# Optimization experiments

Measured on AMD Instinct MI355X. Metric: run time of the kernel, lower is better.

## Reference

```python
import jax, jax.numpy as jnp
import numpy as np
import math

D = 768      # d_model
H = 12       # heads
DH = D // H  # per-head dim
HID = 3072   # ffn hidden
L = 6        # layers each for encoder/decoder
S = 1024     # encoder seq len
T = 1024     # decoder seq len
MAXLEN = 1024


def pos_encoding(d, length):
    # pe[pos, 2i] = sin(pos / scale**i), pe[pos, 2i+1] = cos(pos / scale**i), scale = 1000**(2/d)
    scale = 1000.0 ** (2.0 / d)
    inv = scale ** (-np.arange(d // 2, dtype=np.float64))
    ang = np.arange(length, dtype=np.float64)[:, None] * inv[None, :]
    pe = np.zeros((length, d), dtype=np.float32)
    pe[:, 0::2] = np.sin(ang)
    pe[:, 1::2] = np.cos(ang)
    return jnp.asarray(pe)


def setup_inputs() -> dict:
    key = jax.random.key(0)
    ks = iter(jax.random.split(key, 64))
    def nrm(shape, s=0.02):
        return jax.random.normal(next(ks), shape, dtype=jnp.float32) * s
    inp = {
        'xl': nrm((S, D), 1.0),
        'dl': nrm((T, D), 1.0),
        'pos_enc': pos_encoding(D, MAXLEN),
        # encoder params (stacked over L layers, heads stacked over H)
        'enc_wq': nrm((L, H, DH, D)), 'enc_wk': nrm((L, H, DH, D)), 'enc_wv': nrm((L, H, DH, D)),
        'enc_wo': nrm((L, D, D)), 'enc_bo': jnp.zeros((L, D), jnp.float32),
        'enc_ln_a': jnp.ones((L, 2, D), jnp.float32), 'enc_ln_b': jnp.zeros((L, 2, D), jnp.float32),
        'enc_w1': nrm((L, HID, D)), 'enc_b1': jnp.zeros((L, HID), jnp.float32),
        'enc_w2': nrm((L, D, HID)), 'enc_b2': jnp.zeros((L, D), jnp.float32),
        # decoder self-attention
        'dec_wq': nrm((L, H, DH, D)), 'dec_wk': nrm((L, H, DH, D)), 'dec_wv': nrm((L, H, DH, D)),
        'dec_wo': nrm((L, D, D)), 'dec_bo': jnp.zeros((L, D), jnp.float32),
        # decoder cross-attention
        'dec_cwq': nrm((L, H, DH, D)), 'dec_cwk': nrm((L, H, DH, D)), 'dec_cwv': nrm((L, H, DH, D)),
        'dec_cwo': nrm((L, D, D)), 'dec_cbo': jnp.zeros((L, D), jnp.float32),
        'dec_ln_a': jnp.ones((L, 3, D), jnp.float32), 'dec_ln_b': jnp.zeros((L, 3, D), jnp.float32),
        'dec_w1': nrm((L, HID, D)), 'dec_b1': jnp.zeros((L, HID), jnp.float32),
        'dec_w2': nrm((L, D, HID)), 'dec_b2': jnp.zeros((L, D), jnp.float32),
    }
    return inp


def _ln_res(x, fx, a, b, eps=1e-6):
    # x = x + fx; a*(x-mean)/(std+eps)+b with UNBIASED std (torch default) and std (not var) in denom
    x = x + fx
    m = x.mean(-1, keepdims=True)
    s = jnp.std(x, axis=-1, keepdims=True, ddof=1)
    return a * (x - m) / (s + eps) + b


def _mha(qx, kx, vx, wq, wk, wv, wo, bo, mask=None):
    q = jnp.einsum('sd,hed->hse', qx, wq)  # [H,S,dh]
    k = jnp.einsum('td,hed->hte', kx, wk)
    v = jnp.einsum('td,hed->hte', vx, wv)
    scores = jnp.einsum('hse,hte->hst', q, k) / math.sqrt(q.shape[-1])
    if mask is not None:
        scores = scores + mask
    p = jax.nn.softmax(scores, axis=-1)  # softmax over keys (torch dim=1 on 2D scores)
    o = jnp.einsum('hst,hte->hse', p, v)
    o = jnp.transpose(o, (1, 0, 2)).reshape(qx.shape[0], -1)  # concat heads
    return o @ wo.T + bo


def _ffn(x, w1, b1, w2, b2):
    return jax.nn.relu(x @ w1.T + b1) @ w2.T + b2


def reference(xl, dl, pos_enc, enc_wq, enc_wk, enc_wv, enc_wo, enc_bo, enc_ln_a, enc_ln_b,
              enc_w1, enc_b1, enc_w2, enc_b2,
              dec_wq, dec_wk, dec_wv, dec_wo, dec_bo,
              dec_cwq, dec_cwk, dec_cwv, dec_cwo, dec_cbo,
              dec_ln_a, dec_ln_b, dec_w1, dec_b1, dec_w2, dec_b2):
    m = xl + pos_enc[: xl.shape[0]]
    for l in range(L):
        fx = _mha(m, m, m, enc_wq[l], enc_wk[l], enc_wv[l], enc_wo[l], enc_bo[l])
        m = _ln_res(m, fx, enc_ln_a[l, 0], enc_ln_b[l, 0])
        fx = _ffn(m, enc_w1[l], enc_b1[l], enc_w2[l], enc_b2[l])
        m = _ln_res(m, fx, enc_ln_a[l, 1], enc_ln_b[l, 1])
    n = dl.shape[0]
    # additive causal mask: -10000 where j > i
    cmask = -10000.0 * (jnp.arange(n)[None, :] > jnp.arange(n)[:, None]).astype(jnp.float32)
    out = dl + pos_enc[:n]
    for l in range(L):
        fx = _mha(out, out, out, dec_wq[l], dec_wk[l], dec_wv[l], dec_wo[l], dec_bo[l], cmask)
        out = _ln_res(out, fx, dec_ln_a[l, 0], dec_ln_b[l, 0])
        fx = _mha(out, m, m, dec_cwq[l], dec_cwk[l], dec_cwv[l], dec_cwo[l], dec_cbo[l])
        out = _ln_res(out, fx, dec_ln_a[l, 1], dec_ln_b[l, 1])
        fx = _ffn(out, dec_w1[l], dec_b1[l], dec_w2[l], dec_b2[l])
        out = _ln_res(out, fx, dec_ln_a[l, 2], dec_ln_b[l, 2])
    return jax.nn.softmax(out, axis=1)
```

## Files before the change

### kernel.cpp

```cpp
#include <hip/hip_runtime.h>
#include <math.h>

#define DMODEL 768
#define NHEAD 12
#define DHEAD 64
#define HIDDEN 3072
#define NLAYER 6
#define SEQ 1024
#define AC_ELEMS (SEQ * DMODEL)

typedef unsigned short u16;
typedef __attribute__((ext_vector_type(8))) short short8;
typedef __attribute__((ext_vector_type(4))) float f32x4;

__device__ __forceinline__ u16 f2bf(float f) {
    union { float f; unsigned u; } v; v.f = f;
    unsigned u = v.u;
    return (u16)((u + 0x7fffu + ((u >> 16) & 1u)) >> 16);
}
__device__ __forceinline__ float bf2f(u16 b) {
    union { unsigned u; float f; } v; v.u = ((unsigned)b) << 16; return v.f;
}

__device__ __forceinline__ void async16(const void* g, void* l) {
    __builtin_amdgcn_global_load_lds(
        (const __attribute__((address_space(1))) unsigned int*)g,
        (__attribute__((address_space(3))) unsigned int*)l, 16, 0, 0);
}

template<int N> __device__ __forceinline__ void waitv() {
    asm volatile("s_waitcnt vmcnt(%0)" :: "n"(N) : "memory");
    __builtin_amdgcn_sched_barrier(0);
}
__device__ __forceinline__ void drain_all() {
    asm volatile("s_waitcnt vmcnt(0) lgkmcnt(0)" ::: "memory");
    __builtin_amdgcn_sched_barrier(0);
}
__device__ __forceinline__ void bar() {
    __builtin_amdgcn_sched_barrier(0);
    __builtin_amdgcn_s_barrier();
    __builtin_amdgcn_sched_barrier(0);
}

__device__ __forceinline__ float block_sum(float v, float* red) {
    int tid = threadIdx.x;
    red[tid] = v;
    __syncthreads();
#pragma unroll
    for (int s = 128; s > 0; s >>= 1) {
        if (tid < s) red[tid] += red[tid + s];
        __syncthreads();
    }
    float r = red[0];
    __syncthreads();
    return r;
}
__device__ __forceinline__ float block_max(float v, float* red) {
    int tid = threadIdx.x;
    red[tid] = v;
    __syncthreads();
#pragma unroll
    for (int s = 128; s > 0; s >>= 1) {
        if (tid < s) red[tid] = fmaxf(red[tid], red[tid + s]);
        __syncthreads();
    }
    float r = red[0];
    __syncthreads();
    return r;
}

__global__ __launch_bounds__(256) void add_pe(const float* __restrict__ a,
                                              const float* __restrict__ b,
                                              float* __restrict__ o,
                                              u16* __restrict__ ob, int n) {
    int i = blockIdx.x * 256 + threadIdx.x;
    if (i < n) { float v = a[i] + b[i]; o[i] = v; ob[i] = f2bf(v); }
}

__global__ __launch_bounds__(256) void cvt_bf16(const float* __restrict__ src,
                                                u16* __restrict__ dst,
                                                long long per, long long sls, long long dls) {
    long long i = ((long long)blockIdx.x * 256 + threadIdx.x) * 4;
    if (i >= per) return;
    const float* s = src + (long long)blockIdx.y * sls + i;
    u16* d = dst + (long long)blockIdx.y * dls + i;
    float4 v = *(const float4*)s;
    ushort4 o;
    o.x = f2bf(v.x); o.y = f2bf(v.y); o.z = f2bf(v.z); o.w = f2bf(v.w);
    *(ushort4*)d = o;
}

template<int TM, int TN, int WR, int WC>
__global__ __launch_bounds__(WR * WC * 64) void gemm_mfma(
    const u16* __restrict__ A, int lda,
    const void* __restrict__ Bp, int ldb, int b_f32,
    const float* __restrict__ bias,
    void* __restrict__ Cp, int ldc, int c_bf16,
    float* __restrict__ C2,
    u16* __restrict__ vt_out, int vt_col0,
    int Ksub, int relu)
{
    constexpr int T  = WR * WC * 64;
    constexpr bool MW = (WR * WC) > 1;
    constexpr int FM = TM / (WR * 16), FN = TN / (WC * 16);
    constexpr int NA = TM * 8 / T, NB = TN * 8 / T;
    constexpr int LPS = NA + NB;
    __shared__ __align__(16) u16 As[3][TM * 64];
    __shared__ __align__(16) u16 Bs[3][TN * 64];

    const int zs = blockIdx.z;
    const u16*   B16 = (const u16*)Bp   + (long long)zs * Ksub;
    const float* B32 = (const float*)Bp + (long long)zs * Ksub;
    A += (long long)zs * Ksub;
    u16*   C16 = (u16*)Cp;
    float* C32 = (float*)Cp;

    const int t = threadIdx.x, lane = t & 63, w = t >> 6;
    const int wy = w / WC, wx = w % WC;
    const int n0 = blockIdx.y * TM, m0 = blockIdx.x * TN;

    auto stage = [&](int b, int k0) {
#pragma unroll
        for (int i = 0; i < NA; ++i) {
            int L = i * T + t;
            int row = L >> 3, cp = L & 7, c = cp ^ (row & 7);
            async16(A + (long long)(n0 + row) * lda + k0 + (c << 3),
                    &As[b][(i * T + w * 64) * 8]);
        }
        if (!b_f32) {
#pragma unroll
            for (int i = 0; i < NB; ++i) {
                int L = i * T + t;
                int row = L >> 3, cp = L & 7, c = cp ^ (row & 7);
                async16(B16 + (long long)(m0 + row) * ldb + k0 + (c << 3),
                        &Bs[b][(i * T + w * 64) * 8]);
            }
        } else {
#pragma unroll
            for (int i = 0; i < NB; ++i) {
                int L = i * T + t;
                int row = L >> 3, cp = L & 7, c = cp ^ (row & 7);
                const float* s = B32 + (long long)(m0 + row) * ldb + k0 + (c << 3);
                float4 x = *(const float4*)s;
                float4 y = *(const float4*)(s + 4);
                uint4 pk;
                pk.x = (unsigned)f2bf(x.x) | ((unsigned)f2bf(x.y) << 16);
                pk.y = (unsigned)f2bf(x.z) | ((unsigned)f2bf(x.w) << 16);
                pk.z = (unsigned)f2bf(y.x) | ((unsigned)f2bf(y.y) << 16);
                pk.w = (unsigned)f2bf(y.z) | ((unsigned)f2bf(y.w) << 16);
                *(uint4*)&Bs[b][row * 64 + cp * 8] = pk;
            }
        }
    };

    const int nk = Ksub / 64;
    stage(0, 0);
    if (nk > 1) stage(1, 64);

    f32x4 acc[FM][FN] = {};

    for (int tt = 0; tt < nk; ++tt) {
        if (tt + 2 < nk) stage((tt + 2) % 3, (tt + 2) * 64);
        if (b_f32)             drain_all();
        else if (tt + 2 < nk)  waitv<2 * LPS>();
        else if (tt + 1 < nk)  waitv<LPS>();
        else                   waitv<0>();
        if (MW) bar();

        const u16* Ac = As[tt % 3];
        const u16* Bc = Bs[tt % 3];
#pragma unroll
        for (int kk = 0; kk < 2; ++kk) {
            short8 af[FM], bfv[FN];
            const int cb = kk * 4 + (lane >> 4);
#pragma unroll
            for (int m = 0; m < FM; ++m) {
                int R = wy * (TM / WR) + m * 16 + (lane & 15);
                af[m] = *(const short8*)&Ac[R * 64 + ((cb ^ (R & 7)) << 3)];
            }
#pragma unroll
            for (int n = 0; n < FN; ++n) {
                int R = wx * (TN / WC) + n * 16 + (lane & 15);
                bfv[n] = *(const short8*)&Bc[R * 64 + ((cb ^ (R & 7)) << 3)];
            }
#pragma unroll
            for (int m = 0; m < FM; ++m)
#pragma unroll
                for (int n = 0; n < FN; ++n)
                    acc[m][n] = __builtin_amdgcn_mfma_f32_16x16x32_bf16(af[m], bfv[n], acc[m][n], 0, 0, 0);
        }
        if (MW) bar();
    }

    const int cj = lane & 15, ci0 = (lane >> 4) << 2;
    const bool z0 = (zs == 0);
#pragma unroll
    for (int m = 0; m < FM; ++m) {
#pragma unroll
        for (int n = 0; n < FN; ++n) {
            int col = m0 + wx * (TN / WC) + n * 16 + cj;
            bool to_vt = z0 && vt_out && (col >= vt_col0);
            float bv = (z0 && bias) ? bias[col] : 0.0f;
#pragma unroll
            for (int r = 0; r < 4; ++r) {
                int row = n0 + wy * (TM / WR) + m * 16 + ci0 + r;
                float v = acc[m][n][r] + bv;
                if (relu) v = fmaxf(v, 0.0f);
                if (!z0)          C2[(long long)row * ldc + col] = v;
                else if (to_vt)   vt_out[(long long)(col - vt_col0) * SEQ + row] = f2bf(v);
                else if (c_bf16)  C16[(long long)row * ldc + col] = f2bf(v);
                else              C32[(long long)row * ldc + col] = v;
            }
        }
    }
}

template<int CAUSAL>
__global__ __launch_bounds__(256) void attn_split(
    const u16* __restrict__ Qg,
    const u16* __restrict__ Kg,
    const u16* __restrict__ VT,
    float* __restrict__ Op,
    float* __restrict__ Ml)
{
    const int h  = blockIdx.y;
    const int qt = blockIdx.x;
    const int s  = blockIdx.z;
    const int q0 = qt * 64;
    const int t = threadIdx.x, lane = t & 63, w = t >> 6;

    const int last = CAUSAL ? qt : (SEQ / 64 - 1);

    if (CAUSAL && s > last) {
        for (int e = t; e < 64 * 64; e += 256) {
            int r = e >> 6, c = e & 63;
            Op[(long long)s * AC_ELEMS + (long long)(q0 + r) * DMODEL + h * 64 + c] = 0.0f;
        }
        if (t < 64) {
            long long mi = (((long long)s * NHEAD + h) * SEQ + q0 + t) * 2;
            Ml[mi] = -3.0e38f; Ml[mi + 1] = 0.0f;
        }
        return;
    }

    __shared__ __align__(16) u16 Ks[2][64 * 64];
    __shared__ __align__(16) u16 Vs[2][64 * 64];
    __shared__ __align__(16) u16 Ps[4][16 * 64];

    short8 qf[2];
    {
        int qrow = q0 + w * 16 + (lane & 15);
        const u16* qp = Qg + (long long)qrow * (3 * DMODEL) + h * DHEAD + ((lane >> 4) << 3);
        qf[0] = *(const short8*)qp;
        qf[1] = *(const short8*)(qp + 32);
    }

    auto stage = [&](int b, int kt) {
#pragma unroll
        for (int i = 0; i < 2; ++i) {
            int LL = i * 256 + t;
            int row = LL >> 3, cp = LL & 7, c = cp ^ (row & 7);
            async16(Kg + (long long)(kt * 64 + row) * (3 * DMODEL) + h * DHEAD + (c << 3),
                    &Ks[b][(i * 256 + w * 64) * 8]);
            async16(VT + (long long)(h * DHEAD + row) * SEQ + kt * 64 + (c << 3),
                    &Vs[b][(i * 256 + w * 64) * 8]);
        }
    };

    f32x4 o_acc[4] = {};
    float m_r[4], l_r[4];
#pragma unroll
    for (int r = 0; r < 4; ++r) { m_r[r] = -3.0e38f; l_r[r] = 0.f; }

    stage(0, s);

    int buf = 0;
    for (int kt = s; kt <= last; kt += 2) {
        if (kt + 2 <= last) { stage(buf ^ 1, kt + 2); waitv<4>(); }
        else                { waitv<0>(); }
        bar();

        f32x4 sv[4] = {};
#pragma unroll
        for (int kk = 0; kk < 2; ++kk) {
            const int cb = kk * 4 + (lane >> 4);
#pragma unroll
            for (int n = 0; n < 4; ++n) {
                int R = n * 16 + (lane & 15);
                short8 kf = *(const short8*)&Ks[buf][R * 64 + ((cb ^ (R & 7)) << 3)];
                sv[n] = __builtin_amdgcn_mfma_f32_16x16x32_bf16(qf[kk], kf, sv[n], 0, 0, 0);
            }
        }

#pragma unroll
        for (int n = 0; n < 4; ++n) {
            int keyl = n * 16 + (lane & 15);
#pragma unroll
            for (int r = 0; r < 4; ++r) {
                float v = sv[n][r] * 0.125f;
                if (CAUSAL && kt == qt) {
                    int ql = w * 16 + ((lane >> 4) << 2) + r;
                    if (keyl > ql) v -= 10000.0f;
                }
                sv[n][r] = v;
            }
        }

#pragma unroll
        for (int r = 0; r < 4; ++r) {
            float vm = fmaxf(fmaxf(sv[0][r], sv[1][r]), fmaxf(sv[2][r], sv[3][r]));
            vm = fmaxf(vm, __shfl_xor(vm, 1));
            vm = fmaxf(vm, __shfl_xor(vm, 2));
            vm = fmaxf(vm, __shfl_xor(vm, 4));
            vm = fmaxf(vm, __shfl_xor(vm, 8));
            float mn = fmaxf(m_r[r], vm);
            float sf = __expf(m_r[r] - mn);
            m_r[r] = mn;
            float rowsum = 0.f;
#pragma unroll
            for (int n = 0; n < 4; ++n) {
                float p = __expf(sv[n][r] - mn);
                sv[n][r] = p;
                rowsum += p;
            }
            rowsum += __shfl_xor(rowsum, 1);
            rowsum += __shfl_xor(rowsum, 2);
            rowsum += __shfl_xor(rowsum, 4);
            rowsum += __shfl_xor(rowsum, 8);
            l_r[r] = l_r[r] * sf + rowsum;
#pragma unroll
            for (int d = 0; d < 4; ++d) o_acc[d][r] *= sf;
        }

#pragma unroll
        for (int n = 0; n < 4; ++n) {
            int jh = lane & 7;
            int chunk = n * 2 + ((lane & 15) >> 3);
#pragma unroll
            for (int r = 0; r < 4; ++r) {
                int q = ((lane >> 4) << 2) + r;
                Ps[w][q * 64 + ((chunk ^ (q & 7)) << 3) + jh] = f2bf(sv[n][r]);
            }
        }

#pragma unroll
        for (int kk = 0; kk < 2; ++kk) {
            int q = lane & 15;
            int chunk = (lane >> 4) + kk * 4;
            short8 pf = *(const short8*)&Ps[w][q * 64 + ((chunk ^ (q & 7)) << 3)];
            const int cb = kk * 4 + (lane >> 4);
#pragma unroll
            for (int d = 0; d < 4; ++d) {
                int R = d * 16 + (lane & 15);
                short8 vf = *(const short8*)&Vs[buf][R * 64 + ((cb ^ (R & 7)) << 3)];
                o_acc[d] = __builtin_amdgcn_mfma_f32_16x16x32_bf16(pf, vf, o_acc[d], 0, 0, 0);
            }
        }
        bar();
        buf ^= 1;
    }

#pragma unroll
    for (int r = 0; r < 4; ++r) {
        int row = q0 + w * 16 + ((lane >> 4) << 2) + r;
#pragma unroll
        for (int d = 0; d < 4; ++d) {
            int col = h * DHEAD + d * 16 + (lane & 15);
            Op[(long long)s * AC_ELEMS + (long long)row * DMODEL + col] = o_acc[d][r];
        }
        if ((lane & 15) == 0) {
            long long mi = (((long long)s * NHEAD + h) * SEQ + row) * 2;
            Ml[mi] = m_r[r]; Ml[mi + 1] = l_r[r];
        }
    }
}

__global__ __launch_bounds__(192) void attn_combine(const float* __restrict__ Op,
                                                    const float* __restrict__ Ml,
                                                    u16* __restrict__ O) {
    const int row = blockIdx.x;
    const int c0 = threadIdx.x * 4;
    const int h = c0 >> 6;
    long long m0i = (((long long)0 * NHEAD + h) * SEQ + row) * 2;
    long long m1i = (((long long)1 * NHEAD + h) * SEQ + row) * 2;
    float m0 = Ml[m0i], l0 = Ml[m0i + 1];
    float m1 = Ml[m1i], l1 = Ml[m1i + 1];
    float M = fmaxf(m0, m1);
    float w0 = __expf(m0 - M), w1 = __expf(m1 - M);
    float inv = 1.0f / (w0 * l0 + w1 * l1);
    float4 a = *(const float4*)&Op[(long long)row * DMODEL + c0];
    float4 b = *(const float4*)&Op[(long long)AC_ELEMS + (long long)row * DMODEL + c0];
    ushort4 o;
    o.x = f2bf((w0 * a.x + w1 * b.x) * inv);
    o.y = f2bf((w0 * a.y + w1 * b.y) * inv);
    o.z = f2bf((w0 * a.z + w1 * b.z) * inv);
    o.w = f2bf((w0 * a.w + w1 * b.w) * inv);
    *(ushort4*)&O[(long long)row * DMODEL + c0] = o;
}

__global__ __launch_bounds__(256) void softmax_f32(const float* __restrict__ in,
                                                   float* __restrict__ out, int width) {
    const float* row = in + (long long)blockIdx.x * width;
    float* orow = out + (long long)blockIdx.x * width;
    int tid = threadIdx.x;
    __shared__ float red[256];
    int nf4 = width >> 2;
    float4 v = {-1e30f, -1e30f, -1e30f, -1e30f};
    if (tid < nf4) v = ((const float4*)row)[tid];
    float mx = fmaxf(fmaxf(v.x, v.y), fmaxf(v.z, v.w));
    mx = block_max(mx, red);
    float4 e = {0.f, 0.f, 0.f, 0.f};
    float s = 0.f;
    if (tid < nf4) {
        e.x = __expf(v.x - mx); e.y = __expf(v.y - mx);
        e.z = __expf(v.z - mx); e.w = __expf(v.w - mx);
        s = e.x + e.y + e.z + e.w;
    }
    s = block_sum(s, red);
    float inv = 1.0f / s;
    if (tid < nf4) {
        e.x *= inv; e.y *= inv; e.z *= inv; e.w *= inv;
        ((float4*)orow)[tid] = e;
    }
}

__global__ __launch_bounds__(256) void ln_res_kernel(float* __restrict__ x,
                                                     const float* __restrict__ fx,
                                                     const float* __restrict__ fx2,
                                                     const float* __restrict__ ga,
                                                     const float* __restrict__ gb,
                                                     u16* __restrict__ xb) {
    long long row = blockIdx.x;
    float* xr = x + row * DMODEL;
    const float* fr = fx + row * DMODEL;
    u16* xbr = xb + row * DMODEL;
    int tid = threadIdx.x;
    __shared__ float red[256];

    float4 tv = {0.f, 0.f, 0.f, 0.f};
    if (tid < 192) {
        float4 a = ((const float4*)xr)[tid];
        float4 f = ((const float4*)fr)[tid];
        tv.x = a.x + f.x; tv.y = a.y + f.y; tv.z = a.z + f.z; tv.w = a.w + f.w;
        if (fx2) {
            float4 g = ((const float4*)(fx2 + row * DMODEL))[tid];
            tv.x += g.x; tv.y += g.y; tv.z += g.z; tv.w += g.w;
        }
    }
    float sum = tv.x + tv.y + tv.z + tv.w;
    sum = block_sum(sum, red);
    float mean = sum * (1.0f / (float)DMODEL);

    float4 d = {0.f, 0.f, 0.f, 0.f};
    float ss = 0.f;
    if (tid < 192) {
        d.x = tv.x - mean; d.y = tv.y - mean; d.z = tv.z - mean; d.w = tv.w - mean;
        ss = d.x * d.x + d.y * d.y + d.z * d.z + d.w * d.w;
    }
    ss = block_sum(ss, red);
    float stdv = sqrtf(ss / (float)(DMODEL - 1));
    float inv = 1.0f / (stdv + 1e-6f);

    if (tid < 192) {
        float4 A = ((const float4*)ga)[tid];
        float4 B = ((const float4*)gb)[tid];
        float4 o;
        o.x = A.x * d.x * inv + B.x;
        o.y = A.y * d.y * inv + B.y;
        o.z = A.z * d.z * inv + B.z;
        o.w = A.w * d.w * inv + B.w;
        ((float4*)xr)[tid] = o;
        ushort4 ob;
        ob.x = f2bf(o.x); ob.y = f2bf(o.y); ob.z = f2bf(o.z); ob.w = f2bf(o.w);
        ((ushort4*)xbr)[tid] = ob;
    }
}

struct GArg {
    const u16* A; int lda;
    const void* B; int ldb; int b_f32;
    const float* bias;
    void* C; int ldc; int c_bf16;
    u16* vt; int vt_col0;
    int N, M, K; int relu;
};
template<int TM, int TN, int WR, int WC>
static inline void glaunch(hipStream_t st, const GArg& a, int splitk = 1, float* C2 = nullptr) {
    dim3 grid(a.M / TN, a.N / TM, splitk);
    hipLaunchKernelGGL((gemm_mfma<TM, TN, WR, WC>), grid, dim3(WR * WC * 64), 0, st,
                       a.A, a.lda, a.B, a.ldb, a.b_f32, a.bias, a.C, a.ldc, a.c_bf16,
                       C2, a.vt, a.vt_col0, a.K / splitk, a.relu);
}

extern "C" void kernel_launch(void* const* d_in, const int* in_sizes, int n_in,
                              void* d_out, int out_size, void* d_ws, size_t ws_size,
                              hipStream_t stream) {
    const float* xl      = (const float*)d_in[0];
    const float* dl      = (const float*)d_in[1];
    const float* pe      = (const float*)d_in[2];
    const float* enc_wq  = (const float*)d_in[3];
    const float* enc_wk  = (const float*)d_in[4];
    const float* enc_wv  = (const float*)d_in[5];
    const float* enc_wo  = (const float*)d_in[6];
    const float* enc_bo  = (const float*)d_in[7];
    const float* enc_lna = (const float*)d_in[8];
    const float* enc_lnb = (const float*)d_in[9];
    const float* enc_w1  = (const float*)d_in[10];
    const float* enc_b1  = (const float*)d_in[11];
    const float* enc_w2  = (const float*)d_in[12];
    const float* enc_b2  = (const float*)d_in[13];
    const float* dec_wq  = (const float*)d_in[14];
    const float* dec_wk  = (const float*)d_in[15];
    const float* dec_wv  = (const float*)d_in[16];
    const float* dec_wo  = (const float*)d_in[17];
    const float* dec_bo  = (const float*)d_in[18];
    const float* dec_cwq = (const float*)d_in[19];
    const float* dec_cwk = (const float*)d_in[20];
    const float* dec_cwv = (const float*)d_in[21];
    const float* dec_cwo = (const float*)d_in[22];
    const float* dec_cbo = (const float*)d_in[23];
    const float* dec_lna = (const float*)d_in[24];
    const float* dec_lnb = (const float*)d_in[25];
    const float* dec_w1  = (const float*)d_in[26];
    const float* dec_b1  = (const float*)d_in[27];
    const float* dec_w2  = (const float*)d_in[28];
    const float* dec_b2  = (const float*)d_in[29];

    const long long AC   = AC_ELEMS;
    const long long DD   = (long long)DMODEL * DMODEL;
    const long long WH   = (long long)HIDDEN * DMODEL;
    const long long QKVC = (long long)SEQ * 3 * DMODEL;
    const long long SH   = (long long)SEQ * HIDDEN;

    float* mbuf  = (float*)d_ws;
    float* xbuf  = mbuf + AC;
    float* fbuf  = xbuf + AC;
    float* fbuf2 = fbuf + AC;
    float* Opart = fbuf2 + AC;
    float* Ml    = Opart + 2 * AC;
    u16* u = (u16*)(Ml + 2LL * NHEAD * SEQ * 2);
    u16* mb16 = u;  u += AC;
    u16* xb16 = u;  u += AC;
    u16* qkvb = u;  u += QKVC;
    u16* vt   = u;  u += AC;
    u16* ob   = u;  u += AC;
    u16* hb   = u;  u += SH;

    u16* W = u;
    long long woff = 0;
    const long long W_ENC_QKV = woff; woff += 18 * DD;
    const long long W_ENC_WO  = woff; woff += 6 * DD;
    const long long W_ENC_W1  = woff; woff += 6 * WH;
    const long long W_ENC_W2  = woff; woff += 6 * WH;
    const long long W_DEC_QKV = woff; woff += 18 * DD;
    const long long W_DEC_CQKV= woff; woff += 18 * DD;
    const long long W_DEC_WO  = woff; woff += 6 * DD;
    const long long W_DEC_CWO = woff; woff += 6 * DD;
    const long long W_DEC_W1  = woff; woff += 6 * WH;
    const long long W_DEC_W2  = woff; woff += 6 * WH;
    const long long need = (long long)((char*)(W + woff) - (char*)d_ws);
    const bool conv = ((long long)ws_size >= need);

    if (conv) {
        auto cvt = [&](const float* src, long long dst_off, long long per, long long sls, long long dls, int L) {
            dim3 grid((unsigned)((per / 4 + 255) / 256), L);
            hipLaunchKernelGGL(cvt_bf16, grid, dim3(256), 0, stream, src, W + dst_off, per, sls, dls);
        };
        cvt(enc_wq, W_ENC_QKV + 0 * DD, DD, DD, 3 * DD, NLAYER);
        cvt(enc_wk, W_ENC_QKV + 1 * DD, DD, DD, 3 * DD, NLAYER);
        cvt(enc_wv, W_ENC_QKV + 2 * DD, DD, DD, 3 * DD, NLAYER);
        cvt(enc_wo, W_ENC_WO, 6 * DD, 0, 0, 1);
        cvt(enc_w1, W_ENC_W1, 6 * WH, 0, 0, 1);
        cvt(enc_w2, W_ENC_W2, 6 * WH, 0, 0, 1);
        cvt(dec_wq, W_DEC_QKV + 0 * DD, DD, DD, 3 * DD, NLAYER);
        cvt(dec_wk, W_DEC_QKV + 1 * DD, DD, DD, 3 * DD, NLAYER);
        cvt(dec_wv, W_DEC_QKV + 2 * DD, DD, DD, 3 * DD, NLAYER);
        cvt(dec_cwq, W_DEC_CQKV + 0 * DD, DD, DD, 3 * DD, NLAYER);
        cvt(dec_cwk, W_DEC_CQKV + 1 * DD, DD, DD, 3 * DD, NLAYER);
        cvt(dec_cwv, W_DEC_CQKV + 2 * DD, DD, DD, 3 * DD, NLAYER);
        cvt(dec_wo, W_DEC_WO, 6 * DD, 0, 0, 1);
        cvt(dec_cwo, W_DEC_CWO, 6 * DD, 0, 0, 1);
        cvt(dec_w1, W_DEC_W1, 6 * WH, 0, 0, 1);
        cvt(dec_w2, W_DEC_W2, 6 * WH, 0, 0, 1);
    }

    hipLaunchKernelGGL(add_pe, dim3((int)(AC / 256)), dim3(256), 0, stream, xl, pe, mbuf, mb16, (int)AC);

    auto attn = [&](int causal) {
        dim3 grid(SEQ / 64, NHEAD, 2);
        if (causal)
            hipLaunchKernelGGL((attn_split<1>), grid, dim3(256), 0, stream,
                               qkvb, qkvb + DMODEL, vt, Opart, Ml);
        else
            hipLaunchKernelGGL((attn_split<0>), grid, dim3(256), 0, stream,
                               qkvb, qkvb + DMODEL, vt, Opart, Ml);
        hipLaunchKernelGGL(attn_combine, dim3(SEQ), dim3(192), 0, stream, Opart, Ml, ob);
    };

    for (int l = 0; l < NLAYER; ++l) {
        if (conv) {
            GArg qkv = { mb16, DMODEL, W + W_ENC_QKV + l * 3 * DD, DMODEL, 0, nullptr,
                         qkvb, 3 * DMODEL, 1, vt, 2 * DMODEL, SEQ, 3 * DMODEL, DMODEL, 0 };
            glaunch<64, 64, 2, 2>(stream, qkv);
        } else {
            const float* wps[3] = { enc_wq + l * DD, enc_wk + l * DD, enc_wv + l * DD };
            for (int j = 0; j < 3; ++j) {
                GArg a = { mb16, DMODEL, wps[j], DMODEL, 1, nullptr,
                           qkvb + j * DMODEL, 3 * DMODEL, 1,
                           (j == 2) ? vt : nullptr, 0, SEQ, DMODEL, DMODEL, 0 };
                glaunch<32, 32, 1, 1>(stream, a);
            }
        }
        attn(0);
        GArg wo = { ob, DMODEL,
                    conv ? (const void*)(W + W_ENC_WO + l * DD) : (const void*)(enc_wo + l * DD),
                    DMODEL, conv ? 0 : 1, enc_bo + (long long)l * DMODEL,
                    fbuf, DMODEL, 0, nullptr, 0, SEQ, DMODEL, DMODEL, 0 };
        glaunch<32, 32, 1, 1>(stream, wo);
        hipLaunchKernelGGL(ln_res_kernel, dim3(SEQ), dim3(256), 0, stream,
                           mbuf, fbuf, (const float*)nullptr,
                           enc_lna + (long long)(l * 2 + 0) * DMODEL,
                           enc_lnb + (long long)(l * 2 + 0) * DMODEL, mb16);
        GArg f1 = { mb16, DMODEL,
                    conv ? (const void*)(W + W_ENC_W1 + l * WH) : (const void*)(enc_w1 + l * WH),
                    DMODEL, conv ? 0 : 1, enc_b1 + (long long)l * HIDDEN,
                    hb, HIDDEN, 1, nullptr, 0, SEQ, HIDDEN, DMODEL, 1 };
        glaunch<64, 64, 2, 2>(stream, f1);
        GArg f2 = { hb, HIDDEN,
                    conv ? (const void*)(W + W_ENC_W2 + l * WH) : (const void*)(enc_w2 + l * WH),
                    HIDDEN, conv ? 0 : 1, enc_b2 + (long long)l * DMODEL,
                    fbuf, DMODEL, 0, nullptr, 0, SEQ, DMODEL, HIDDEN, 0 };
        glaunch<64, 64, 2, 2>(stream, f2, 2, fbuf2);
        hipLaunchKernelGGL(ln_res_kernel, dim3(SEQ), dim3(256), 0, stream,
                           mbuf, fbuf, fbuf2,
                           enc_lna + (long long)(l * 2 + 1) * DMODEL,
                           enc_lnb + (long long)(l * 2 + 1) * DMODEL, mb16);
    }

    hipLaunchKernelGGL(add_pe, dim3((int)(AC / 256)), dim3(256), 0, stream, dl, pe, xbuf, xb16, (int)AC);

    for (int l = 0; l < NLAYER; ++l) {
        if (conv) {
            GArg qkv = { xb16, DMODEL, W + W_DEC_QKV + l * 3 * DD, DMODEL, 0, nullptr,
                         qkvb, 3 * DMODEL, 1, vt, 2 * DMODEL, SEQ, 3 * DMODEL, DMODEL, 0 };
            glaunch<64, 64, 2, 2>(stream, qkv);
        } else {
            const float* wps[3] = { dec_wq + l * DD, dec_wk + l * DD, dec_wv + l * DD };
            for (int j = 0; j < 3; ++j) {
                GArg a = { xb16, DMODEL, wps[j], DMODEL, 1, nullptr,
                           qkvb + j * DMODEL, 3 * DMODEL, 1,
                           (j == 2) ? vt : nullptr, 0, SEQ, DMODEL, DMODEL, 0 };
                glaunch<32, 32, 1, 1>(stream, a);
            }
        }
        attn(1);
        GArg wo = { ob, DMODEL,
                    conv ? (const void*)(W + W_DEC_WO + l * DD) : (const void*)(dec_wo + l * DD),
                    DMODEL, conv ? 0 : 1, dec_bo + (long long)l * DMODEL,
                    fbuf, DMODEL, 0, nullptr, 0, SEQ, DMODEL, DMODEL, 0 };
        glaunch<32, 32, 1, 1>(stream, wo);
        hipLaunchKernelGGL(ln_res_kernel, dim3(SEQ), dim3(256), 0, stream,
                           xbuf, fbuf, (const float*)nullptr,
                           dec_lna + (long long)(l * 3 + 0) * DMODEL,
                           dec_lnb + (long long)(l * 3 + 0) * DMODEL, xb16);

        if (conv) {
            GArg q = { xb16, DMODEL, W + W_DEC_CQKV + l * 3 * DD, DMODEL, 0, nullptr,
                       qkvb, 3 * DMODEL, 1, nullptr, 0, SEQ, DMODEL, DMODEL, 0 };
            glaunch<32, 32, 1, 1>(stream, q);
            GArg kv = { mb16, DMODEL, W + W_DEC_CQKV + l * 3 * DD + DD, DMODEL, 0, nullptr,
                        qkvb + DMODEL, 3 * DMODEL, 1, vt, DMODEL, SEQ, 2 * DMODEL, DMODEL, 0 };
            glaunch<32, 32, 1, 1>(stream, kv);
        } else {
            GArg q = { xb16, DMODEL, dec_cwq + l * DD, DMODEL, 1, nullptr,
                       qkvb, 3 * DMODEL, 1, nullptr, 0, SEQ, DMODEL, DMODEL, 0 };
            glaunch<32, 32, 1, 1>(stream, q);
            GArg ck = { mb16, DMODEL, dec_cwk + l * DD, DMODEL, 1, nullptr,
                        qkvb + DMODEL, 3 * DMODEL, 1, nullptr, 0, SEQ, DMODEL, DMODEL, 0 };
            glaunch<32, 32, 1, 1>(stream, ck);
            GArg cv = { mb16, DMODEL, dec_cwv + l * DD, DMODEL, 1, nullptr,
                        qkvb + 2 * DMODEL, 3 * DMODEL, 1, vt, 0, SEQ, DMODEL, DMODEL, 0 };
            glaunch<32, 32, 1, 1>(stream, cv);
        }
        attn(0);
        GArg cwo = { ob, DMODEL,
                     conv ? (const void*)(W + W_DEC_CWO + l * DD) : (const void*)(dec_cwo + l * DD),
                     DMODEL, conv ? 0 : 1, dec_cbo + (long long)l * DMODEL,
                     fbuf, DMODEL, 0, nullptr, 0, SEQ, DMODEL, DMODEL, 0 };
        glaunch<32, 32, 1, 1>(stream, cwo);
        hipLaunchKernelGGL(ln_res_kernel, dim3(SEQ), dim3(256), 0, stream,
                           xbuf, fbuf, (const float*)nullptr,
                           dec_lna + (long long)(l * 3 + 1) * DMODEL,
                           dec_lnb + (long long)(l * 3 + 1) * DMODEL, xb16);

        GArg f1 = { xb16, DMODEL,
                    conv ? (const void*)(W + W_DEC_W1 + l * WH) : (const void*)(dec_w1 + l * WH),
                    DMODEL, conv ? 0 : 1, dec_b1 + (long long)l * HIDDEN,
                    hb, HIDDEN, 1, nullptr, 0, SEQ, HIDDEN, DMODEL, 1 };
        glaunch<64, 64, 2, 2>(stream, f1);
        GArg f2 = { hb, HIDDEN,
                    conv ? (const void*)(W + W_DEC_W2 + l * WH) : (const void*)(dec_w2 + l * WH),
                    HIDDEN, conv ? 0 : 1, dec_b2 + (long long)l * DMODEL,
                    fbuf, DMODEL, 0, nullptr, 0, SEQ, DMODEL, HIDDEN, 0 };
        glaunch<64, 64, 2, 2>(stream, f2, 2, fbuf2);
        hipLaunchKernelGGL(ln_res_kernel, dim3(SEQ), dim3(256), 0, stream,
                           xbuf, fbuf, fbuf2,
                           dec_lna + (long long)(l * 3 + 2) * DMODEL,
                           dec_lnb + (long long)(l * 3 + 2) * DMODEL, xb16);
    }

    hipLaunchKernelGGL(softmax_f32, dim3(SEQ), dim3(256), 0, stream, xbuf, (float*)d_out, DMODEL);
}
```

Baseline: 1.750 ms.

## Widen GEMM tiles, add XCD-aware block swizzle, deepen FFN2 split-K to four

Adds an XCD-aware remap of workgroup indices so neighbouring tiles land on the same chiplet and share L2. Enlarges the GEMM tiles from 64x64 to 64x128 for the QKV, FFN and cross-attention KV projections. Raises the FFN2 split-K from 2 to 4, with each extra slice written to its own partial buffer and the LayerNorm kernel summing the three partials. The larger tiles and swizzle aim to cut redundant global loads, and the deeper split-K restores parallelism lost to fewer blocks. In exchange it costs extra partial-buffer traffic and more workspace.

```diff
diff --git a/kernel.cpp b/kernel.cpp
--- a/kernel.cpp
+++ b/kernel.cpp
@@ -40,6 +40,17 @@
     __builtin_amdgcn_sched_barrier(0);
     __builtin_amdgcn_s_barrier();
     __builtin_amdgcn_sched_barrier(0);
+}
+
+__device__ __forceinline__ void xcd_swz(int& bx, int& by) {
+    const int gx = gridDim.x;
+    const int nwg = gx * gridDim.y;
+    int orig = by * gx + bx;
+    if ((nwg & 7) == 0) {
+        int wg = (orig & 7) * (nwg >> 3) + (orig >> 3);
+        bx = wg % gx;
+        by = wg / gx;
+    }
 }
 
 __device__ __forceinline__ float block_sum(float v, float* red) {
@@ -108,6 +119,9 @@
     __shared__ __align__(16) u16 As[3][TM * 64];
     __shared__ __align__(16) u16 Bs[3][TN * 64];
 
+    int bx = blockIdx.x, by = blockIdx.y;
+    xcd_swz(bx, by);
+
     const int zs = blockIdx.z;
     const u16*   B16 = (const u16*)Bp   + (long long)zs * Ksub;
     const float* B32 = (const float*)Bp + (long long)zs * Ksub;
@@ -117,7 +131,7 @@
 
     const int t = threadIdx.x, lane = t & 63, w = t >> 6;
     const int wy = w / WC, wx = w % WC;
-    const int n0 = blockIdx.y * TM, m0 = blockIdx.x * TN;
+    const int n0 = by * TM, m0 = bx * TN;
 
     auto stage = [&](int b, int k0) {
 #pragma unroll
@@ -194,6 +208,7 @@
 
     const int cj = lane & 15, ci0 = (lane >> 4) << 2;
     const bool z0 = (zs == 0);
+    float* C2z = C2 + (long long)(zs - 1) * AC_ELEMS;
 #pragma unroll
     for (int m = 0; m < FM; ++m) {
 #pragma unroll
@@ -206,7 +221,7 @@
                 int row = n0 + wy * (TM / WR) + m * 16 + ci0 + r;
                 float v = acc[m][n][r] + bv;
                 if (relu) v = fmaxf(v, 0.0f);
-                if (!z0)          C2[(long long)row * ldc + col] = v;
+                if (!z0)          C2z[(long long)row * ldc + col] = v;
                 else if (to_vt)   vt_out[(long long)(col - vt_col0) * SEQ + row] = f2bf(v);
                 else if (c_bf16)  C16[(long long)row * ldc + col] = f2bf(v);
                 else              C32[(long long)row * ldc + col] = v;
@@ -427,6 +442,7 @@
 __global__ __launch_bounds__(256) void ln_res_kernel(float* __restrict__ x,
                                                      const float* __restrict__ fx,
                                                      const float* __restrict__ fx2,
+                                                     int n2,
                                                      const float* __restrict__ ga,
                                                      const float* __restrict__ gb,
                                                      u16* __restrict__ xb) {
@@ -442,8 +458,8 @@
         float4 a = ((const float4*)xr)[tid];
         float4 f = ((const float4*)fr)[tid];
         tv.x = a.x + f.x; tv.y = a.y + f.y; tv.z = a.z + f.z; tv.w = a.w + f.w;
-        if (fx2) {
-            float4 g = ((const float4*)(fx2 + row * DMODEL))[tid];
+        for (int j = 0; j < n2; ++j) {
+            float4 g = ((const float4*)(fx2 + (long long)j * AC_ELEMS + row * DMODEL))[tid];
             tv.x += g.x; tv.y += g.y; tv.z += g.z; tv.w += g.w;
         }
     }
@@ -536,7 +552,7 @@
     float* xbuf  = mbuf + AC;
     float* fbuf  = xbuf + AC;
     float* fbuf2 = fbuf + AC;
-    float* Opart = fbuf2 + AC;
+    float* Opart = fbuf2 + 3 * AC;
     float* Ml    = Opart + 2 * AC;
     u16* u = (u16*)(Ml + 2LL * NHEAD * SEQ * 2);
     u16* mb16 = u;  u += AC;
@@ -601,7 +617,7 @@
         if (conv) {
             GArg qkv = { mb16, DMODEL, W + W_ENC_QKV + l * 3 * DD, DMODEL, 0, nullptr,
                          qkvb, 3 * DMODEL, 1, vt, 2 * DMODEL, SEQ, 3 * DMODEL, DMODEL, 0 };
-            glaunch<64, 64, 2, 2>(stream, qkv);
+            glaunch<64, 128, 2, 2>(stream, qkv);
         } else {
             const float* wps[3] = { enc_wq + l * DD, enc_wk + l * DD, enc_wv + l * DD };
             for (int j = 0; j < 3; ++j) {
@@ -618,21 +634,21 @@
                     fbuf, DMODEL, 0, nullptr, 0, SEQ, DMODEL, DMODEL, 0 };
         glaunch<32, 32, 1, 1>(stream, wo);
         hipLaunchKernelGGL(ln_res_kernel, dim3(SEQ), dim3(256), 0, stream,
-                           mbuf, fbuf, (const float*)nullptr,
+                           mbuf, fbuf, (const float*)nullptr, 0,
                            enc_lna + (long long)(l * 2 + 0) * DMODEL,
                            enc_lnb + (long long)(l * 2 + 0) * DMODEL, mb16);
         GArg f1 = { mb16, DMODEL,
                     conv ? (const void*)(W + W_ENC_W1 + l * WH) : (const void*)(enc_w1 + l * WH),
                     DMODEL, conv ? 0 : 1, enc_b1 + (long long)l * HIDDEN,
                     hb, HIDDEN, 1, nullptr, 0, SEQ, HIDDEN, DMODEL, 1 };
-        glaunch<64, 64, 2, 2>(stream, f1);
+        glaunch<64, 128, 2, 2>(stream, f1);
         GArg f2 = { hb, HIDDEN,
                     conv ? (const void*)(W + W_ENC_W2 + l * WH) : (const void*)(enc_w2 + l * WH),
                     HIDDEN, conv ? 0 : 1, enc_b2 + (long long)l * DMODEL,
                     fbuf, DMODEL, 0, nullptr, 0, SEQ, DMODEL, HIDDEN, 0 };
-        glaunch<64, 64, 2, 2>(stream, f2, 2, fbuf2);
+        glaunch<64, 128, 2, 2>(stream, f2, 4, fbuf2);
         hipLaunchKernelGGL(ln_res_kernel, dim3(SEQ), dim3(256), 0, stream,
-                           mbuf, fbuf, fbuf2,
+                           mbuf, fbuf, fbuf2, 3,
                            enc_lna + (long long)(l * 2 + 1) * DMODEL,
                            enc_lnb + (long long)(l * 2 + 1) * DMODEL, mb16);
     }
@@ -643,7 +659,7 @@
         if (conv) {
             GArg qkv = { xb16, DMODEL, W + W_DEC_QKV + l * 3 * DD, DMODEL, 0, nullptr,
                          qkvb, 3 * DMODEL, 1, vt, 2 * DMODEL, SEQ, 3 * DMODEL, DMODEL, 0 };
-            glaunch<64, 64, 2, 2>(stream, qkv);
+            glaunch<64, 128, 2, 2>(stream, qkv);
         } else {
             const float* wps[3] = { dec_wq + l * DD, dec_wk + l * DD, dec_wv + l * DD };
             for (int j = 0; j < 3; ++j) {
@@ -660,7 +676,7 @@
                     fbuf, DMODEL, 0, nullptr, 0, SEQ, DMODEL, DMODEL, 0 };
         glaunch<32, 32, 1, 1>(stream, wo);
         hipLaunchKernelGGL(ln_res_kernel, dim3(SEQ), dim3(256), 0, stream,
-                           xbuf, fbuf, (const float*)nullptr,
+                           xbuf, fbuf, (const float*)nullptr, 0,
                            dec_lna + (long long)(l * 3 + 0) * DMODEL,
                            dec_lnb + (long long)(l * 3 + 0) * DMODEL, xb16);
 
@@ -670,7 +686,7 @@
             glaunch<32, 32, 1, 1>(stream, q);
             GArg kv = { mb16, DMODEL, W + W_DEC_CQKV + l * 3 * DD + DD, DMODEL, 0, nullptr,
                         qkvb + DMODEL, 3 * DMODEL, 1, vt, DMODEL, SEQ, 2 * DMODEL, DMODEL, 0 };
-            glaunch<32, 32, 1, 1>(stream, kv);
+            glaunch<64, 128, 2, 2>(stream, kv);
         } else {
             GArg q = { xb16, DMODEL, dec_cwq + l * DD, DMODEL, 1, nullptr,
                        qkvb, 3 * DMODEL, 1, nullptr, 0, SEQ, DMODEL, DMODEL, 0 };
@@ -689,7 +705,7 @@
                      fbuf, DMODEL, 0, nullptr, 0, SEQ, DMODEL, DMODEL, 0 };
         glaunch<32, 32, 1, 1>(stream, cwo);
         hipLaunchKernelGGL(ln_res_kernel, dim3(SEQ), dim3(256), 0, stream,
-                           xbuf, fbuf, (const float*)nullptr,
+                           xbuf, fbuf, (const float*)nullptr, 0,
                            dec_lna + (long long)(l * 3 + 1) * DMODEL,
                            dec_lnb + (long long)(l * 3 + 1) * DMODEL, xb16);
 
@@ -697,14 +713,14 @@
                     conv ? (const void*)(W + W_DEC_W1 + l * WH) : (const void*)(dec_w1 + l * WH),
                     DMODEL, conv ? 0 : 1, dec_b1 + (long long)l * HIDDEN,
                     hb, HIDDEN, 1, nullptr, 0, SEQ, HIDDEN, DMODEL, 1 };
-        glaunch<64, 64, 2, 2>(stream, f1);
+        glaunch<64, 128, 2, 2>(stream, f1);
         GArg f2 = { hb, HIDDEN,
                     conv ? (const void*)(W + W_DEC_W2 + l * WH) : (const void*)(dec_w2 + l * WH),
                     HIDDEN, conv ? 0 : 1, dec_b2 + (long long)l * DMODEL,
                     fbuf, DMODEL, 0, nullptr, 0, SEQ, DMODEL, HIDDEN, 0 };
-        glaunch<64, 64, 2, 2>(stream, f2, 2, fbuf2);
+        glaunch<64, 128, 2, 2>(stream, f2, 4, fbuf2);
         hipLaunchKernelGGL(ln_res_kernel, dim3(SEQ), dim3(256), 0, stream,
-                           xbuf, fbuf, fbuf2,
+                           xbuf, fbuf, fbuf2, 3,
                            dec_lna + (long long)(l * 3 + 2) * DMODEL,
                            dec_lnb + (long long)(l * 3 + 2) * DMODEL, xb16);
     }
```

Result: slower. 1.810 ms (+3.4%).
